# Kernel tuning notes

Measured on AMD Instinct MI355X. Metric: run time of the kernel, lower is better.

Reference implementation:

```python
import math
import jax, jax.numpy as jnp
import numpy as np

E = 1024   # embedding_dim
H = 16     # nheads
S = 1024   # sequence length (dim 0 of x)
B = 8      # batch (dim 1 of x)
NEG = -1e9


def setup_inputs() -> dict:
    key = jax.random.key(0)
    k0, k1, k2, k3, k4, k5 = jax.random.split(key, 6)
    x = jax.random.normal(k0, (S, B, E), dtype=jnp.float32)
    mask = jax.random.randint(k1, (B, S), 0, 2, dtype=jnp.int32)
    # nn.Linear params: y = x @ W.T + b, init scale ~ 1/sqrt(fan_in)
    s = 1.0 / math.sqrt(E)
    qkv_w = jax.random.uniform(k2, (3 * E, E), jnp.float32, -s, s)
    qkv_b = jax.random.uniform(k3, (3 * E,), jnp.float32, -s, s)
    out_w = jax.random.uniform(k4, (E, E), jnp.float32, -s, s)
    out_b = jax.random.uniform(k5, (E,), jnp.float32, -s, s)
    return {"x": x, "mask": mask, "qkv_w": qkv_w, "qkv_b": qkv_b,
            "out_w": out_w, "out_b": out_b}


def reference(x, mask, qkv_w, qkv_b, out_w, out_b):
    # x: (S, B, E); mask: (B, S) int -> .float() in torch
    Dh = E // H
    scale = math.sqrt(E / H)

    qkv = x @ qkv_w.T + qkv_b                      # (S, B, 3E)
    q, k, v = jnp.split(qkv, 3, axis=-1)           # each (S, B, E)

    # (S, B, E) -> (S, B*H, Dh) -> (B*H, S, Dh)
    q = q.reshape(S, B * H, Dh).transpose(1, 0, 2) / scale
    k = k.reshape(S, B * H, Dh).transpose(1, 2, 0)  # (B*H, Dh, S)
    v = v.reshape(S, B * H, Dh).transpose(1, 0, 2)  # (B*H, S, Dh)

    m = jnp.repeat(mask.astype(jnp.float32), H, axis=0)  # (B*H, S)
    q = q * m[:, :, None]
    k = k * m[None - 0, :, None].transpose(0, 2, 1) if False else k * m[:, None, :]
    m2 = m[:, :, None] * m[:, None, :]                   # (B*H, S, S)

    # baddbmm(1 - m2, q, k, beta=-1e9) = -1e9*(1 - m2) + q @ k
    attn = NEG * (1.0 - m2) + jnp.matmul(q, k)           # (B*H, S, S)
    attn = jax.nn.softmax(attn, axis=-1)

    o = jnp.matmul(attn, v)                              # (B*H, S, Dh)
    o = o.transpose(1, 0, 2).reshape(S, B, E)
    o = o @ out_w.T + out_b                              # (S, B, E)
    # dropout is identity in eval mode
    attn = attn.reshape(B, H, S, S)
    return o, attn
```

## Files before the change

kernel.cpp:

```cpp
#include <hip/hip_runtime.h>
#include <hip/hip_bf16.h>
#include <stdint.h>

#define S_ 1024
#define B_ 8
#define E_ 1024
#define H_ 16
#define DH_ 64
#define NHEAD_ 128

typedef __bf16 bf16;
typedef bf16 bf16x8 __attribute__((ext_vector_type(8)));
typedef bf16 bf16x4 __attribute__((ext_vector_type(4)));
typedef float fx4 __attribute__((ext_vector_type(4)));

static __device__ __forceinline__ fx4 mfma_bf16(bf16x8 a, bf16x8 b, fx4 c) {
  return __builtin_amdgcn_mfma_f32_16x16x32_bf16(a, b, c, 0, 0, 0);
}

static __device__ __forceinline__ void gload16(const void* g, void* lds) {
  __builtin_amdgcn_global_load_lds(
      (const __attribute__((address_space(1))) unsigned int*)g,
      (__attribute__((address_space(3))) unsigned int*)lds, 16, 0, 0);
}

__global__ __launch_bounds__(256) void k_cast(const float* __restrict__ src,
                                              bf16* __restrict__ dst, int n8) {
  int i = blockIdx.x * 256 + threadIdx.x;
  if (i >= n8) return;
  const fx4* s4 = (const fx4*)src;
  fx4 a = s4[2 * i], b = s4[2 * i + 1];
  bf16x8 o;
  o[0] = (bf16)a[0]; o[1] = (bf16)a[1]; o[2] = (bf16)a[2]; o[3] = (bf16)a[3];
  o[4] = (bf16)b[0]; o[5] = (bf16)b[1]; o[6] = (bf16)b[2]; o[7] = (bf16)b[3];
  ((bf16x8*)dst)[i] = o;
}

template <int MODE>
__global__ __launch_bounds__(256) void k_gemm(const bf16* __restrict__ A,
                                              const bf16* __restrict__ W,
                                              const float* __restrict__ bias, int K,
                                              bf16* __restrict__ Qg, bf16* __restrict__ Kg,
                                              bf16* __restrict__ Vt, float* __restrict__ Cout) {
  __shared__ __align__(16) bf16 As[128 * 32];
  __shared__ __align__(16) bf16 Bs[128 * 32];
  const int tid = threadIdx.x;
  const int l = tid & 63, w = tid >> 6;
  const int r16 = l & 15, kg = l >> 4;
  const int row0 = blockIdx.x * 128, col0 = blockIdx.y * 128;
  const int wm = (w >> 1) * 64, wn = (w & 1) * 64;

  fx4 acc[4][4];
#pragma unroll
  for (int i = 0; i < 4; i++)
#pragma unroll
    for (int j = 0; j < 4; j++) acc[i][j] = (fx4){0.f, 0.f, 0.f, 0.f};

  const int rA = w * 16 + (l >> 2);
  const int srcoff = (((l & 3) ^ ((rA >> 1) & 3)) * 8);
  const size_t gA0 = (size_t)(row0 + rA) * K + srcoff;
  const size_t gA1 = (size_t)(row0 + rA + 64) * K + srcoff;
  const size_t gB0 = (size_t)(col0 + rA) * K + srcoff;
  const size_t gB1 = (size_t)(col0 + rA + 64) * K + srcoff;
  char* ldsA = (char*)As + w * 1024;
  char* ldsB = (char*)Bs + w * 1024;

  for (int k0 = 0; k0 < K; k0 += 32) {
    gload16(A + gA0 + k0, ldsA);
    gload16(A + gA1 + k0, ldsA + 4096);
    gload16(W + gB0 + k0, ldsB);
    gload16(W + gB1 + k0, ldsB + 4096);
    __syncthreads();
    bf16x8 af[4], bfr[4];
#pragma unroll
    for (int i = 0; i < 4; i++) {
      int r = wm + i * 16 + r16;
      af[i] = *(const bf16x8*)((char*)As + r * 64 + ((kg ^ ((r >> 1) & 3)) * 16));
    }
#pragma unroll
    for (int j = 0; j < 4; j++) {
      int r = wn + j * 16 + r16;
      bfr[j] = *(const bf16x8*)((char*)Bs + r * 64 + ((kg ^ ((r >> 1) & 3)) * 16));
    }
#pragma unroll
    for (int i = 0; i < 4; i++)
#pragma unroll
      for (int j = 0; j < 4; j++) acc[i][j] = mfma_bf16(af[i], bfr[j], acc[i][j]);
    __syncthreads();
  }

#pragma unroll
  for (int j = 0; j < 4; j++) {
    const int cg = col0 + wn + j * 16 + r16;
    const float bs = bias[cg];
    if (MODE == 0) {
      const int sec = cg >> 10;
      const int e = cg & 1023;
      const int h = e >> 6, dh = e & 63;
#pragma unroll
      for (int i = 0; i < 4; i++) {
#pragma unroll
        for (int t = 0; t < 4; t++) {
          const int rg = row0 + wm + i * 16 + kg * 4 + t;
          const int s = rg >> 3, bb = rg & 7;
          const int head = bb * 16 + h;
          const float v = acc[i][j][t] + bs;
          if (sec == 0)
            Qg[((size_t)head * 1024 + s) * 64 + dh] = (bf16)(v * 0.125f);
          else if (sec == 1)
            Kg[((size_t)head * 1024 + s) * 64 + dh] = (bf16)v;
          else
            Vt[((size_t)head * 64 + dh) * 1024 + s] = (bf16)v;
        }
      }
    } else {
#pragma unroll
      for (int i = 0; i < 4; i++)
#pragma unroll
        for (int t = 0; t < 4; t++) {
          const int rg = row0 + wm + i * 16 + kg * 4 + t;
          Cout[(size_t)rg * 1024 + cg] = acc[i][j][t] + bs;
        }
    }
  }
}

__global__ __launch_bounds__(256) void k_attn(const bf16* __restrict__ Qg,
                                              const bf16* __restrict__ Kg,
                                              const bf16* __restrict__ Vt,
                                              const int* __restrict__ mask,
                                              float* __restrict__ attn_out,
                                              bf16* __restrict__ o_mid) {
  __shared__ __align__(16) bf16 P[16 * 1024];
  __shared__ float mm[1024];
  __shared__ float rinv[16];
  __shared__ int mrow[16];

  const int tid = threadIdx.x;
  const int l = tid & 63, w = tid >> 6;
  const int r16 = l & 15, kg = l >> 4;
  const int head = blockIdx.x >> 6;
  const int q0 = (blockIdx.x & 63) << 4;
  const int b = head >> 4;
  const int h = head & 15;

  for (int i = tid; i < 1024; i += 256) mm[i] = mask[b * 1024 + i] ? 1.0f : 0.0f;
  if (tid < 16) mrow[tid] = mask[b * 1024 + q0 + tid];
  __syncthreads();

  const bf16* qp = Qg + ((size_t)head * 1024 + q0 + r16) * 64 + kg * 8;
  const bf16x8 aq0 = *(const bf16x8*)qp;
  const bf16x8 aq1 = *(const bf16x8*)(qp + 32);

#pragma unroll 4
  for (int t = 0; t < 16; t++) {
    const int key0 = w * 256 + t * 16;
    const bf16* kp = Kg + ((size_t)head * 1024 + key0 + r16) * 64 + kg * 8;
    bf16x8 b0 = *(const bf16x8*)kp;
    bf16x8 b1 = *(const bf16x8*)(kp + 32);
    fx4 c = {0.f, 0.f, 0.f, 0.f};
    c = mfma_bf16(aq0, b0, c);
    c = mfma_bf16(aq1, b1, c);
    const int key = key0 + r16;
    const float mj = mm[key];
#pragma unroll
    for (int e = 0; e < 4; e++) {
      const int row = kg * 4 + e;
      const float p = __expf(c[e]) * mj;
      *(bf16*)((char*)P + row * 2048 + ((key * 2) ^ ((row & 7) << 4))) = (bf16)p;
    }
  }
  __syncthreads();

  {
    const int r = tid >> 4, c16 = tid & 15;
    if (mrow[r] == 0) {
      bf16x8 f;
#pragma unroll
      for (int j = 0; j < 8; j++) f[j] = (bf16)0.0009765625f;
#pragma unroll
      for (int i = 0; i < 8; i++) {
        const int unit = c16 * 8 + i;
        *(bf16x8*)((char*)P + r * 2048 + ((unit ^ (r & 7)) << 4)) = f;
      }
    }
  }
  __syncthreads();

#pragma unroll
  for (int rr = 0; rr < 4; rr++) {
    const int row = w * 4 + rr;
    const int xr = row & 7;
    bf16x8 v0 = *(const bf16x8*)((char*)P + row * 2048 + (((2 * l) ^ xr) << 4));
    bf16x8 v1 = *(const bf16x8*)((char*)P + row * 2048 + (((2 * l + 1) ^ xr) << 4));
    float s = 0.f;
#pragma unroll
    for (int j = 0; j < 8; j++) s += (float)v0[j] + (float)v1[j];
#pragma unroll
    for (int off = 32; off >= 1; off >>= 1) s += __shfl_xor(s, off, 64);
    if (l == 0) rinv[row] = 1.0f / s;
  }
  __syncthreads();

  {
    const int r = tid >> 4, c16 = tid & 15;
    const float ri = rinv[r];
    float* op = attn_out + ((size_t)(head * 1024) + q0 + r) * 1024;
#pragma unroll
    for (int i = 0; i < 16; i++) {
      const int key = c16 * 4 + i * 64;
      bf16x4 pv = *(const bf16x4*)((char*)P + r * 2048 + ((key * 2) ^ ((r & 7) << 4)));
      fx4 o;
      o[0] = (float)pv[0] * ri;
      o[1] = (float)pv[1] * ri;
      o[2] = (float)pv[2] * ri;
      o[3] = (float)pv[3] * ri;
      *(fx4*)(op + key) = o;
    }
  }

  {
    fx4 c = {0.f, 0.f, 0.f, 0.f};
    const bf16* vp = Vt + ((size_t)head * 64 + w * 16 + r16) * 1024 + kg * 8;
#pragma unroll 4
    for (int kt = 0; kt < 32; kt++) {
      bf16x8 a = *(const bf16x8*)((char*)P + r16 * 2048 +
                                  ((kt * 64 + kg * 16) ^ ((r16 & 7) << 4)));
      bf16x8 bv = *(const bf16x8*)(vp + kt * 32);
      c = mfma_bf16(a, bv, c);
    }
#pragma unroll
    for (int e = 0; e < 4; e++) {
      const int qrow = kg * 4 + e;
      const float val = c[e] * rinv[qrow];
      o_mid[((size_t)(q0 + qrow) * 8 + b) * 1024 + h * 64 + w * 16 + r16] = (bf16)val;
    }
  }
}

extern "C" void kernel_launch(void* const* d_in, const int* in_sizes, int n_in,
                              void* d_out, int out_size, void* d_ws, size_t ws_size,
                              hipStream_t stream) {
  const float* x = (const float*)d_in[0];
  const int* mask = (const int*)d_in[1];
  const float* qkv_w = (const float*)d_in[2];
  const float* qkv_b = (const float*)d_in[3];
  const float* out_w = (const float*)d_in[4];
  const float* out_b = (const float*)d_in[5];

  float* out_o = (float*)d_out;
  float* out_attn = out_o + (size_t)S_ * B_ * E_;

  char* ws = (char*)d_ws;
  bf16* x_bf = (bf16*)(ws);
  bf16* wqkv_bf = (bf16*)(ws + (16ull << 20));
  bf16* wout_bf = (bf16*)(ws + (22ull << 20));
  bf16* Qg = (bf16*)(ws + (24ull << 20));
  bf16* Kg = (bf16*)(ws + (40ull << 20));
  bf16* Vt = (bf16*)(ws + (56ull << 20));
  bf16* o_mid = (bf16*)(ws + (72ull << 20));

  k_cast<<<4096, 256, 0, stream>>>(x, x_bf, 1048576);
  k_cast<<<1536, 256, 0, stream>>>(qkv_w, wqkv_bf, 393216);
  k_cast<<<512, 256, 0, stream>>>(out_w, wout_bf, 131072);

  dim3 g1(64, 24);
  k_gemm<0><<<g1, 256, 0, stream>>>(x_bf, wqkv_bf, qkv_b, 1024, Qg, Kg, Vt, nullptr);

  k_attn<<<8192, 256, 0, stream>>>(Qg, Kg, Vt, mask, out_attn, o_mid);

  dim3 g2(64, 8);
  k_gemm<1><<<g2, 256, 0, stream>>>(o_mid, wout_bf, out_b, 1024, nullptr, nullptr, nullptr, out_o);
}
```

Before: 922.7 us.

## Fold softmax scale into weights, fuse row sums, remap blocks, vectorize attention stores

Folds the 1/8 scale and log2(e) into the Q weights and bias so the attention kernel uses exp2 directly. Row sums are built during the exp pass with shuffles, which removes a full LDS reread and one barrier. Swapped MFMA operands let each lane pack four P or output values with v_cvt_pk_bf16 and store them together, and the attn_out writes become wider. Also adds 1D grid swizzles for GEMM and attention blocks (XCD/L2 locality), s_setprio around MFMAs, and launch_bounds occupancy hint; risks slight numeric differences from the bf16 rounding of the scaled Q weights.

After: 958.7 us. 3.9% more time.

```diff
diff --git a/kernel.cpp b/kernel.cpp
--- a/kernel.cpp
+++ b/kernel.cpp
@@ -6,13 +6,13 @@
 #define B_ 8
 #define E_ 1024
 #define H_ 16
-#define DH_ 64
-#define NHEAD_ 128
 
 typedef __bf16 bf16;
 typedef bf16 bf16x8 __attribute__((ext_vector_type(8)));
-typedef bf16 bf16x4 __attribute__((ext_vector_type(4)));
 typedef float fx4 __attribute__((ext_vector_type(4)));
+typedef uint32_t u32x2 __attribute__((ext_vector_type(2)));
+
+#define QSCALE 0.18033688011112042f
 
 static __device__ __forceinline__ fx4 mfma_bf16(bf16x8 a, bf16x8 b, fx4 c) {
   return __builtin_amdgcn_mfma_f32_16x16x32_bf16(a, b, c, 0, 0, 0);
@@ -24,15 +24,25 @@
       (__attribute__((address_space(3))) unsigned int*)lds, 16, 0, 0);
 }
 
+static __device__ __forceinline__ uint32_t cvtpk(float lo, float hi) {
+  uint32_t r;
+  asm("v_cvt_pk_bf16_f32 %0, %1, %2" : "=v"(r) : "v"(lo), "v"(hi));
+  return r;
+}
+
 __global__ __launch_bounds__(256) void k_cast(const float* __restrict__ src,
-                                              bf16* __restrict__ dst, int n8) {
+                                              bf16* __restrict__ dst, int n8,
+                                              int limit8, float scale) {
   int i = blockIdx.x * 256 + threadIdx.x;
   if (i >= n8) return;
+  const float sc = (i < limit8) ? scale : 1.0f;
   const fx4* s4 = (const fx4*)src;
   fx4 a = s4[2 * i], b = s4[2 * i + 1];
   bf16x8 o;
-  o[0] = (bf16)a[0]; o[1] = (bf16)a[1]; o[2] = (bf16)a[2]; o[3] = (bf16)a[3];
-  o[4] = (bf16)b[0]; o[5] = (bf16)b[1]; o[6] = (bf16)b[2]; o[7] = (bf16)b[3];
+  o[0] = (bf16)(a[0] * sc); o[1] = (bf16)(a[1] * sc);
+  o[2] = (bf16)(a[2] * sc); o[3] = (bf16)(a[3] * sc);
+  o[4] = (bf16)(b[0] * sc); o[5] = (bf16)(b[1] * sc);
+  o[6] = (bf16)(b[2] * sc); o[7] = (bf16)(b[3] * sc);
   ((bf16x8*)dst)[i] = o;
 }
 
@@ -47,7 +57,11 @@
   const int tid = threadIdx.x;
   const int l = tid & 63, w = tid >> 6;
   const int r16 = l & 15, kg = l >> 4;
-  const int row0 = blockIdx.x * 128, col0 = blockIdx.y * 128;
+  const int bid = (int)blockIdx.x;
+  const int ii = bid >> 3;
+  const int bx = (bid & 7) * 8 + (ii & 7);
+  const int by = ii >> 3;
+  const int row0 = bx * 128, col0 = by * 128;
   const int wm = (w >> 1) * 64, wn = (w & 1) * 64;
 
   fx4 acc[4][4];
@@ -82,19 +96,22 @@
       int r = wn + j * 16 + r16;
       bfr[j] = *(const bf16x8*)((char*)Bs + r * 64 + ((kg ^ ((r >> 1) & 3)) * 16));
     }
+    __builtin_amdgcn_s_setprio(1);
 #pragma unroll
     for (int i = 0; i < 4; i++)
 #pragma unroll
       for (int j = 0; j < 4; j++) acc[i][j] = mfma_bf16(af[i], bfr[j], acc[i][j]);
+    __builtin_amdgcn_s_setprio(0);
     __syncthreads();
   }
 
 #pragma unroll
   for (int j = 0; j < 4; j++) {
     const int cg = col0 + wn + j * 16 + r16;
-    const float bs = bias[cg];
+    float bs = bias[cg];
     if (MODE == 0) {
       const int sec = cg >> 10;
+      if (sec == 0) bs *= QSCALE;
       const int e = cg & 1023;
       const int h = e >> 6, dh = e & 63;
 #pragma unroll
@@ -106,7 +123,7 @@
           const int head = bb * 16 + h;
           const float v = acc[i][j][t] + bs;
           if (sec == 0)
-            Qg[((size_t)head * 1024 + s) * 64 + dh] = (bf16)(v * 0.125f);
+            Qg[((size_t)head * 1024 + s) * 64 + dh] = (bf16)v;
           else if (sec == 1)
             Kg[((size_t)head * 1024 + s) * 64 + dh] = (bf16)v;
           else
@@ -125,51 +142,65 @@
   }
 }
 
-__global__ __launch_bounds__(256) void k_attn(const bf16* __restrict__ Qg,
-                                              const bf16* __restrict__ Kg,
-                                              const bf16* __restrict__ Vt,
-                                              const int* __restrict__ mask,
-                                              float* __restrict__ attn_out,
-                                              bf16* __restrict__ o_mid) {
+__global__ __launch_bounds__(256, 4) void k_attn(const bf16* __restrict__ Qg,
+                                                 const bf16* __restrict__ Kg,
+                                                 const bf16* __restrict__ Vt,
+                                                 const int* __restrict__ mask,
+                                                 float* __restrict__ attn_out,
+                                                 bf16* __restrict__ o_mid) {
   __shared__ __align__(16) bf16 P[16 * 1024];
-  __shared__ float mm[1024];
+  __shared__ __align__(16) float mm[1024];
+  __shared__ float psum[16][4];
   __shared__ float rinv[16];
   __shared__ int mrow[16];
 
   const int tid = threadIdx.x;
   const int l = tid & 63, w = tid >> 6;
   const int r16 = l & 15, kg = l >> 4;
-  const int head = blockIdx.x >> 6;
-  const int q0 = (blockIdx.x & 63) << 4;
-  const int b = head >> 4;
-  const int h = head & 15;
+  const int bid = (int)blockIdx.x;
+  const int lb = (bid & 7) * 1024 + (bid >> 3);
+  const int head = lb >> 6;
+  const int q0 = (lb & 63) << 4;
+  const int b = head >> 4, h = head & 15;
 
   for (int i = tid; i < 1024; i += 256) mm[i] = mask[b * 1024 + i] ? 1.0f : 0.0f;
   if (tid < 16) mrow[tid] = mask[b * 1024 + q0 + tid];
   __syncthreads();
 
   const bf16* qp = Qg + ((size_t)head * 1024 + q0 + r16) * 64 + kg * 8;
-  const bf16x8 aq0 = *(const bf16x8*)qp;
-  const bf16x8 aq1 = *(const bf16x8*)(qp + 32);
+  const bf16x8 bq0 = *(const bf16x8*)qp;
+  const bf16x8 bq1 = *(const bf16x8*)(qp + 32);
+
+  const int xr = (r16 & 7) << 4;
+  const int prow = r16 * 2048;
+  float lsum = 0.f;
 
 #pragma unroll 4
   for (int t = 0; t < 16; t++) {
     const int key0 = w * 256 + t * 16;
     const bf16* kp = Kg + ((size_t)head * 1024 + key0 + r16) * 64 + kg * 8;
-    bf16x8 b0 = *(const bf16x8*)kp;
-    bf16x8 b1 = *(const bf16x8*)(kp + 32);
+    bf16x8 a0 = *(const bf16x8*)kp;
+    bf16x8 a1 = *(const bf16x8*)(kp + 32);
     fx4 c = {0.f, 0.f, 0.f, 0.f};
-    c = mfma_bf16(aq0, b0, c);
-    c = mfma_bf16(aq1, b1, c);
-    const int key = key0 + r16;
-    const float mj = mm[key];
-#pragma unroll
-    for (int e = 0; e < 4; e++) {
-      const int row = kg * 4 + e;
-      const float p = __expf(c[e]) * mj;
-      *(bf16*)((char*)P + row * 2048 + ((key * 2) ^ ((row & 7) << 4))) = (bf16)p;
-    }
-  }
+    __builtin_amdgcn_s_setprio(1);
+    c = mfma_bf16(a0, bq0, c);
+    c = mfma_bf16(a1, bq1, c);
+    __builtin_amdgcn_s_setprio(0);
+    const int k4 = key0 + kg * 4;
+    const fx4 m4 = *(const fx4*)&mm[k4];
+    const float p0 = exp2f(c[0]) * m4[0];
+    const float p1 = exp2f(c[1]) * m4[1];
+    const float p2 = exp2f(c[2]) * m4[2];
+    const float p3 = exp2f(c[3]) * m4[3];
+    lsum += (p0 + p1) + (p2 + p3);
+    u32x2 pk;
+    pk[0] = cvtpk(p0, p1);
+    pk[1] = cvtpk(p2, p3);
+    *(u32x2*)((char*)P + prow + ((k4 * 2) ^ xr)) = pk;
+  }
+  lsum += __shfl_xor(lsum, 16, 64);
+  lsum += __shfl_xor(lsum, 32, 64);
+  if (l < 16) psum[l][w] = lsum;
   __syncthreads();
 
   {
@@ -178,44 +209,34 @@
       bf16x8 f;
 #pragma unroll
       for (int j = 0; j < 8; j++) f[j] = (bf16)0.0009765625f;
-#pragma unroll
-      for (int i = 0; i < 8; i++) {
-        const int unit = c16 * 8 + i;
-        *(bf16x8*)((char*)P + r * 2048 + ((unit ^ (r & 7)) << 4)) = f;
-      }
-    }
-  }
-  __syncthreads();
-
-#pragma unroll
-  for (int rr = 0; rr < 4; rr++) {
-    const int row = w * 4 + rr;
-    const int xr = row & 7;
-    bf16x8 v0 = *(const bf16x8*)((char*)P + row * 2048 + (((2 * l) ^ xr) << 4));
-    bf16x8 v1 = *(const bf16x8*)((char*)P + row * 2048 + (((2 * l + 1) ^ xr) << 4));
-    float s = 0.f;
-#pragma unroll
-    for (int j = 0; j < 8; j++) s += (float)v0[j] + (float)v1[j];
-#pragma unroll
-    for (int off = 32; off >= 1; off >>= 1) s += __shfl_xor(s, off, 64);
-    if (l == 0) rinv[row] = 1.0f / s;
+      const int xrr = (r & 7) << 4;
+#pragma unroll
+      for (int i = 0; i < 8; i++)
+        *(bf16x8*)((char*)P + r * 2048 + ((c16 * 16 + i * 256) ^ xrr)) = f;
+    }
+  }
+  if (tid < 16) {
+    const float s = (psum[tid][0] + psum[tid][1]) + (psum[tid][2] + psum[tid][3]);
+    rinv[tid] = mrow[tid] ? 1.0f / s : 1.0f;
   }
   __syncthreads();
 
   {
     const int r = tid >> 4, c16 = tid & 15;
     const float ri = rinv[r];
-    float* op = attn_out + ((size_t)(head * 1024) + q0 + r) * 1024;
-#pragma unroll
-    for (int i = 0; i < 16; i++) {
-      const int key = c16 * 4 + i * 64;
-      bf16x4 pv = *(const bf16x4*)((char*)P + r * 2048 + ((key * 2) ^ ((r & 7) << 4)));
-      fx4 o;
-      o[0] = (float)pv[0] * ri;
-      o[1] = (float)pv[1] * ri;
-      o[2] = (float)pv[2] * ri;
-      o[3] = (float)pv[3] * ri;
-      *(fx4*)(op + key) = o;
+    const int xrr = (r & 7) << 4;
+    float* op = attn_out + ((size_t)head * 1024 + q0 + r) * 1024;
+#pragma unroll
+    for (int i = 0; i < 8; i++) {
+      const int key = i * 128 + c16 * 8;
+      bf16x8 pv = *(const bf16x8*)((char*)P + r * 2048 + ((key * 2) ^ xrr));
+      fx4 o0, o1;
+      o0[0] = (float)pv[0] * ri; o0[1] = (float)pv[1] * ri;
+      o0[2] = (float)pv[2] * ri; o0[3] = (float)pv[3] * ri;
+      o1[0] = (float)pv[4] * ri; o1[1] = (float)pv[5] * ri;
+      o1[2] = (float)pv[6] * ri; o1[3] = (float)pv[7] * ri;
+      *(fx4*)(op + key) = o0;
+      *(fx4*)(op + key + 4) = o1;
     }
   }
 
@@ -224,17 +245,17 @@
     const bf16* vp = Vt + ((size_t)head * 64 + w * 16 + r16) * 1024 + kg * 8;
 #pragma unroll 4
     for (int kt = 0; kt < 32; kt++) {
-      bf16x8 a = *(const bf16x8*)((char*)P + r16 * 2048 +
-                                  ((kt * 64 + kg * 16) ^ ((r16 & 7) << 4)));
-      bf16x8 bv = *(const bf16x8*)(vp + kt * 32);
-      c = mfma_bf16(a, bv, c);
-    }
-#pragma unroll
-    for (int e = 0; e < 4; e++) {
-      const int qrow = kg * 4 + e;
-      const float val = c[e] * rinv[qrow];
-      o_mid[((size_t)(q0 + qrow) * 8 + b) * 1024 + h * 64 + w * 16 + r16] = (bf16)val;
-    }
+      bf16x8 a = *(const bf16x8*)(vp + kt * 32);
+      bf16x8 bp = *(const bf16x8*)((char*)P + r16 * 2048 + ((kt * 64 + kg * 16) ^ xr));
+      __builtin_amdgcn_s_setprio(1);
+      c = mfma_bf16(a, bp, c);
+      __builtin_amdgcn_s_setprio(0);
+    }
+    const float ri = rinv[r16];
+    u32x2 pk;
+    pk[0] = cvtpk(c[0] * ri, c[1] * ri);
+    pk[1] = cvtpk(c[2] * ri, c[3] * ri);
+    *(u32x2*)&o_mid[((size_t)(q0 + r16) * 8 + b) * 1024 + h * 64 + w * 16 + kg * 4] = pk;
   }
 }
 
@@ -260,15 +281,13 @@
   bf16* Vt = (bf16*)(ws + (56ull << 20));
   bf16* o_mid = (bf16*)(ws + (72ull << 20));
 
-  k_cast<<<4096, 256, 0, stream>>>(x, x_bf, 1048576);
-  k_cast<<<1536, 256, 0, stream>>>(qkv_w, wqkv_bf, 393216);
-  k_cast<<<512, 256, 0, stream>>>(out_w, wout_bf, 131072);
-
-  dim3 g1(64, 24);
-  k_gemm<0><<<g1, 256, 0, stream>>>(x_bf, wqkv_bf, qkv_b, 1024, Qg, Kg, Vt, nullptr);
+  k_cast<<<4096, 256, 0, stream>>>(x, x_bf, 1048576, 0, 1.0f);
+  k_cast<<<1536, 256, 0, stream>>>(qkv_w, wqkv_bf, 393216, 131072, QSCALE);
+  k_cast<<<512, 256, 0, stream>>>(out_w, wout_bf, 131072, 0, 1.0f);
+
+  k_gemm<0><<<1536, 256, 0, stream>>>(x_bf, wqkv_bf, qkv_b, 1024, Qg, Kg, Vt, nullptr);
 
   k_attn<<<8192, 256, 0, stream>>>(Qg, Kg, Vt, mask, out_attn, o_mid);
 
-  dim3 g2(64, 8);
-  k_gemm<1><<<g2, 256, 0, stream>>>(o_mid, wout_bf, out_b, 1024, nullptr, nullptr, nullptr, out_o);
-}
+  k_gemm<1><<<512, 256, 0, stream>>>(o_mid, wout_bf, out_b, 1024, nullptr, nullptr, nullptr, out_o);
+}
```
